# Performance work log

Hardware: AMD Instinct MI355X
Metric: run time of the kernel (lower is better)

The kernel has to match this reference:

```python
import jax, jax.numpy as jnp
import numpy as np

C1, C2, C3 = 64, 256, 256
HEADS, WS = 8, 7
HD = C3 // HEADS
PAD = WS // 2
SCALE = HD ** -0.5
EPS = 1e-5


def _layernorm(x, gamma, beta):
    mu = jnp.mean(x, axis=-1, keepdims=True)
    var = jnp.var(x, axis=-1, keepdims=True)
    return (x - mu) * jax.lax.rsqrt(var + EPS) * gamma + beta


def setup_inputs() -> dict:
    key = jax.random.key(0)
    ks = jax.random.split(key, 12)
    B, H, W = 2, 200, 200
    s = 0.02
    return {
        "F_lidar": jax.random.normal(ks[0], (B, C1, H, W), jnp.float32),
        "F_cam": jax.random.normal(ks[1], (B, C2, H, W), jnp.float32),
        "Wq": jax.random.normal(ks[2], (C3, C1), jnp.float32) * s,
        "Wk": jax.random.normal(ks[3], (C3, C2), jnp.float32) * s,
        "Wv": jax.random.normal(ks[4], (C3, C2), jnp.float32) * s,
        "Wo": jax.random.normal(ks[5], (C3, C3), jnp.float32) * s,
        "Wr": jax.random.normal(ks[6], (C3, C1), jnp.float32) * s,
        "g1": jnp.ones((C3,), jnp.float32),
        "b1": jnp.zeros((C3,), jnp.float32),
        "g2": jnp.ones((C3,), jnp.float32),
        "b2": jnp.zeros((C3,), jnp.float32),
        "W1": jax.random.normal(ks[7], (C3, 4 * C3), jnp.float32) * s,
        "bf1": jnp.zeros((4 * C3,), jnp.float32),
        "W2": jax.random.normal(ks[8], (4 * C3, C3), jnp.float32) * s,
        "bf2": jnp.zeros((C3,), jnp.float32),
    }


def reference(F_lidar, F_cam, Wq, Wk, Wv, Wo, Wr, g1, b1, g2, b2, W1, bf1, W2, bf2):
    B, _, H, W = F_lidar.shape
    # 1x1 conv projections (no bias)
    Q = jnp.einsum('oc,bchw->bohw', Wq, F_lidar)
    K = jnp.einsum('oc,bchw->bohw', Wk, F_cam)
    V = jnp.einsum('oc,bchw->bohw', Wv, F_cam)
    # replicate padding (torch 'replicate' == jnp 'edge')
    Kp = jnp.pad(K, ((0, 0), (0, 0), (PAD, PAD), (PAD, PAD)), mode='edge')
    Vp = jnp.pad(V, ((0, 0), (0, 0), (PAD, PAD), (PAD, PAD)), mode='edge')
    Qm = Q.reshape(B, HEADS, HD, H, W)
    # local-window attention logits without materializing the unfolded (C*49) tensor:
    # loop over the 49 fixed window offsets, accumulating per-offset dot products.
    logits = []
    for i in range(WS):
        for j in range(WS):
            Km = Kp[:, :, i:i + H, j:j + W].reshape(B, HEADS, HD, H, W)
            logits.append(jnp.einsum('bndhw,bndhw->bnhw', Qm, Km))
    logits = jnp.stack(logits, axis=-1) * SCALE          # (B, heads, H, W, 49)
    attn = jax.nn.softmax(logits, axis=-1)
    out = jnp.zeros_like(Qm)
    k = 0
    for i in range(WS):
        for j in range(WS):
            Vm = Vp[:, :, i:i + H, j:j + W].reshape(B, HEADS, HD, H, W)
            out = out + attn[..., k][:, :, None] * Vm
            k += 1
    out = out.reshape(B, C3, H, W)
    out = jnp.einsum('oc,bchw->bohw', Wo, out)
    residual = jnp.einsum('oc,bchw->bohw', Wr, F_lidar)
    x = (residual + out).transpose(0, 2, 3, 1)           # (B, H, W, C3)
    x = _layernorm(x, g1, b1)
    # FFN (dropout is identity in eval)
    y = jax.nn.relu(jnp.dot(x, W1) + bf1)
    y = jnp.dot(y, W2) + bf2
    x = _layernorm(x + y, g2, b2)
    return x.transpose(0, 3, 1, 2)
```

## Files before the change

### kernel.cpp

```cpp
#include <hip/hip_runtime.h>
#include <stdint.h>

#define HH 200
#define WW 200
#define HWSZ 40000
#define NPX 80000

typedef __attribute__((ext_vector_type(8))) short bf16x8;
typedef __attribute__((ext_vector_type(4))) float f32x4;

__device__ __forceinline__ float bf2f(unsigned short u) {
    union { uint32_t i; float f; } c; c.i = ((uint32_t)u) << 16; return c.f;
}
__device__ __forceinline__ unsigned short f2bf(float f) {
    union { float f; uint32_t i; } c; c.f = f;
    uint32_t r = c.i + 0x7FFF + ((c.i >> 16) & 1);
    return (unsigned short)(r >> 16);
}
__device__ __forceinline__ unsigned int cvtpk_bf16(float lo, float hi) {
    unsigned int r;
    asm("v_cvt_pk_bf16_f32 %0, %1, %2" : "=v"(r) : "v"(lo), "v"(hi));
    return r;
}

__global__ __launch_bounds__(256) void cvt_weights(
    const float* __restrict__ Wq, const float* __restrict__ Wk,
    const float* __restrict__ Wv, const float* __restrict__ Wo,
    const float* __restrict__ Wr, const float* __restrict__ W1,
    const float* __restrict__ W2,
    unsigned short* Wq_b, unsigned short* Wk_b, unsigned short* Wv_b,
    unsigned short* Wcat, unsigned short* W1t, unsigned short* W2t)
{
    const int seg = blockIdx.y;
    const int idx = blockIdx.x * 256 + threadIdx.x;
    if (seg == 0)      { if (idx < 16384) Wq_b[idx] = f2bf(Wq[idx]); }
    else if (seg == 1) { if (idx < 65536) Wk_b[idx] = f2bf(Wk[idx]); }
    else if (seg == 2) { if (idx < 65536) Wv_b[idx] = f2bf(Wv[idx]); }
    else if (seg == 3) {
        if (idx < 81920) {
            int r = idx / 320, k = idx - r * 320;
            Wcat[idx] = f2bf(k < 256 ? Wo[r * 256 + k] : Wr[r * 64 + (k - 256)]);
        }
    } else if (seg == 4) {
        if (idx < 262144) { int o = idx >> 8, i = idx & 255; W1t[idx] = f2bf(W1[i * 1024 + o]); }
    } else {
        if (idx < 262144) { int o = idx >> 10, i = idx & 1023; W2t[idx] = f2bf(W2[i * 256 + o]); }
    }
}

__global__ __launch_bounds__(256) void to_nhwc(
    const float* __restrict__ src, unsigned short* __restrict__ dst, int C)
{
    __shared__ unsigned short T[64][72];
    const int b = blockIdx.z, c0 = blockIdx.y * 64, px0 = blockIdx.x * 64;
    const int t = threadIdx.x;
    const int pxl = t & 63, cl0 = t >> 6;
    const float* sp = src + ((size_t)(b * C + c0 + cl0)) * HWSZ + px0 + pxl;
    #pragma unroll
    for (int i = 0; i < 16; ++i)
        T[pxl][cl0 + i * 4] = f2bf(sp[(size_t)i * 4 * HWSZ]);
    __syncthreads();
    #pragma unroll
    for (int r = 0; r < 2; ++r) {
        int idx = t + r * 256;
        int p = idx >> 3, cof = (idx & 7) * 8;
        uint4 v = *(const uint4*)&T[p][cof];
        *(uint4*)(dst + ((size_t)(b * HWSZ + px0 + p)) * C + c0 + cof) = v;
    }
}

__global__ __launch_bounds__(256) void gemm_bf16(
    const unsigned short* __restrict__ In, int inStride,
    const unsigned short* __restrict__ In2, int in2Stride, int K1,
    const unsigned short* __restrict__ Wb, int wStride, int Ktot,
    unsigned short* __restrict__ OutB, float* __restrict__ OutF,
    const float* __restrict__ bias, int flags, int outStride)
{
    __shared__ bf16x8 AB[1024];
    const int t = threadIdx.x;
    const int px0 = blockIdx.x * 128;
    const int n0 = blockIdx.y * 128;
    const int lane = t & 63, w = t >> 6;
    const int mh = w & 1, nh = w >> 1;

    f32x4 acc[4][4] = {};

    for (int k0 = 0; k0 < Ktot; k0 += 32) {
        #pragma unroll
        for (int r = 0; r < 2; ++r) {
            const int c = t + r * 256;
            const int l = c & 63;
            const int ko = k0 + ((l >> 4) << 3);
            {
                const int mt = c >> 6;
                const int px = px0 + mt * 16 + (l & 15);
                const unsigned short* sp = (ko < K1)
                    ? (In  + (size_t)px * inStride  + ko)
                    : (In2 + (size_t)px * in2Stride + (ko - K1));
                AB[c] = *(const bf16x8*)sp;
            }
            {
                const int nt = c >> 6;
                const int cc = n0 + nt * 16 + (l & 15);
                AB[512 + c] = *(const bf16x8*)(Wb + (size_t)cc * wStride + ko);
            }
        }
        __syncthreads();
        bf16x8 av[4], bv[4];
        #pragma unroll
        for (int i = 0; i < 4; ++i) av[i] = AB[(mh * 4 + i) * 64 + lane];
        #pragma unroll
        for (int j = 0; j < 4; ++j) bv[j] = AB[512 + (nh * 4 + j) * 64 + lane];
        #pragma unroll
        for (int i = 0; i < 4; ++i)
            #pragma unroll
            for (int j = 0; j < 4; ++j)
                acc[i][j] = __builtin_amdgcn_mfma_f32_16x16x32_bf16(
                    av[i], bv[j], acc[i][j], 0, 0, 0);
        __syncthreads();
    }

    const int q = lane >> 4, ln = lane & 15;
    const bool relu = (flags & 1) != 0, accum = (flags & 2) != 0;
    #pragma unroll
    for (int i = 0; i < 4; ++i) {
        #pragma unroll
        for (int j = 0; j < 4; ++j) {
            const int coutv = n0 + nh * 64 + j * 16 + ln;
            const float bval = bias ? bias[coutv] : 0.0f;
            #pragma unroll
            for (int r = 0; r < 4; ++r) {
                const int px = px0 + mh * 64 + i * 16 + q * 4 + r;
                float v = acc[i][j][r] + bval;
                if (relu) v = fmaxf(v, 0.0f);
                if (OutB) {
                    OutB[(size_t)px * outStride + coutv] = f2bf(v);
                } else {
                    float* op = OutF + (size_t)px * 256 + coutv;
                    if (accum) v += *op;
                    *op = v;
                }
            }
        }
    }
}

__global__ __launch_bounds__(512) void ffn2_ln2(
    const unsigned short* __restrict__ Y1,
    const unsigned short* __restrict__ XLb,
    const unsigned short* __restrict__ W2t,
    const float* __restrict__ bf2v,
    const float* __restrict__ g2, const float* __restrict__ b2,
    float* __restrict__ Out)
{
    __shared__ union {
        bf16x8 AB[1536];
        float  T[256 * 33];
    } sm;
    __shared__ float part_s[4][128], part_q[4][128];

    const int t = threadIdx.x;
    const int px0 = blockIdx.x * 128;
    const int lane = t & 63, w = t >> 6;
    const int mh = w & 1, nh = w >> 1;
    const int q = lane >> 4, ln = lane & 15;

    f32x4 acc[4][4] = {};

    for (int k0 = 0; k0 < 1024; k0 += 32) {
        #pragma unroll
        for (int r = 0; r < 3; ++r) {
            const int c = t + r * 512;
            const int l = c & 63;
            const int ko = k0 + ((l >> 4) << 3);
            if (c < 512) {
                const int mt = c >> 6;
                const int px = px0 + mt * 16 + (l & 15);
                sm.AB[c] = *(const bf16x8*)(Y1 + (size_t)px * 1024 + ko);
            } else {
                const int c2 = c - 512;
                const int nt = c2 >> 6;
                const int cc = nt * 16 + (l & 15);
                sm.AB[c] = *(const bf16x8*)(W2t + (size_t)cc * 1024 + ko);
            }
        }
        __syncthreads();
        bf16x8 av[4], bv[4];
        #pragma unroll
        for (int i = 0; i < 4; ++i) av[i] = sm.AB[(mh * 4 + i) * 64 + lane];
        #pragma unroll
        for (int j = 0; j < 4; ++j) bv[j] = sm.AB[512 + (nh * 4 + j) * 64 + lane];
        #pragma unroll
        for (int i = 0; i < 4; ++i)
            #pragma unroll
            for (int j = 0; j < 4; ++j)
                acc[i][j] = __builtin_amdgcn_mfma_f32_16x16x32_bf16(
                    av[i], bv[j], acc[i][j], 0, 0, 0);
        __syncthreads();
    }

    float biasv[4], gv[4], bvv[4];
    #pragma unroll
    for (int j = 0; j < 4; ++j) {
        const int col = nh * 64 + j * 16 + ln;
        biasv[j] = bf2v[col];
        gv[j] = g2[col];
        bvv[j] = b2[col];
    }

    #pragma unroll
    for (int i = 0; i < 4; ++i) {
        #pragma unroll
        for (int r = 0; r < 4; ++r) {
            const int pl = mh * 64 + i * 16 + q * 4 + r;
            const size_t px = (size_t)px0 + pl;
            float s = 0.0f, ssq = 0.0f;
            #pragma unroll
            for (int j = 0; j < 4; ++j) {
                const int col = nh * 64 + j * 16 + ln;
                float v = acc[i][j][r] + biasv[j] + bf2f(XLb[px * 256 + col]);
                acc[i][j][r] = v;
                s += v; ssq += v * v;
            }
            #pragma unroll
            for (int o = 1; o <= 8; o <<= 1) {
                s += __shfl_xor(s, o); ssq += __shfl_xor(ssq, o);
            }
            if (ln == 0) { part_s[nh][pl] = s; part_q[nh][pl] = ssq; }
        }
    }
    __syncthreads();

    float muv[4][4], rsv[4][4];
    #pragma unroll
    for (int i = 0; i < 4; ++i) {
        #pragma unroll
        for (int r = 0; r < 4; ++r) {
            const int pl = mh * 64 + i * 16 + q * 4 + r;
            const float s  = part_s[0][pl] + part_s[1][pl] + part_s[2][pl] + part_s[3][pl];
            const float sq = part_q[0][pl] + part_q[1][pl] + part_q[2][pl] + part_q[3][pl];
            const float mu = s * (1.0f / 256.0f);
            muv[i][r] = mu;
            rsv[i][r] = rsqrtf(sq * (1.0f / 256.0f) - mu * mu + 1e-5f);
        }
    }
    __syncthreads();

    #pragma unroll
    for (int ck = 0; ck < 4; ++ck) {
        if (mh == (ck >> 1)) {
            const int ib = (ck & 1) * 2;
            #pragma unroll
            for (int ii = 0; ii < 2; ++ii) {
                const int i = ib + ii;
                #pragma unroll
                for (int j = 0; j < 4; ++j) {
                    const int col = nh * 64 + j * 16 + ln;
                    #pragma unroll
                    for (int r = 0; r < 4; ++r) {
                        sm.T[col * 33 + ii * 16 + q * 4 + r] =
                            (acc[i][j][r] - muv[i][r]) * rsv[i][r] * gv[j] + bvv[j];
                    }
                }
            }
        }
        __syncthreads();
        const int pxc = px0 + ck * 32;
        const int bb = pxc / HWSZ;
        const int hw0 = pxc - bb * HWSZ;
        #pragma unroll
        for (int p = 0; p < 16; ++p) {
            const int idx = t + p * 512;
            const int c = idx >> 5, pxl = idx & 31;
            Out[((size_t)(bb * 256 + c)) * HWSZ + hw0 + pxl] = sm.T[c * 33 + pxl];
        }
        __syncthreads();
    }
}

__global__ __launch_bounds__(256) void attn_bf16(
    const unsigned short* Q, const unsigned short* __restrict__ K,
    const unsigned short* __restrict__ V, unsigned short* A)
{
    __shared__ __align__(16) unsigned short vt[32 * 536];
    const int b = blockIdx.z, head = blockIdx.y;
    const int tiy = blockIdx.x / 13, tix = blockIdx.x % 13;
    const int h0 = tiy * 16, w0 = tix * 16;
    const int t = threadIdx.x;
    const int lane = t & 63, wv = t >> 6;
    const int g = lane >> 4, n = lane & 15;
    const int co = head * 32;
    const size_t pxb = (size_t)b * HWSZ;

    for (int idx = t; idx < 832; idx += 256) {
        if (idx < 704) {
            int ch = idx / 22, r = idx - ch * 22;
            *(unsigned int*)&vt[ch * 536 + r * 24 + 22] = 0u;
        } else {
            int k2 = idx - 704;
            int ch = k2 >> 2, e = k2 & 3;
            *(unsigned int*)&vt[ch * 536 + 528 + e * 2] = 0u;
        }
    }
    for (int idx = t; idx < 484 * 4; idx += 256) {
        int pos = idx >> 2, chunk = idx & 3;
        int r = pos / 22, c = pos - r * 22;
        int gh = min(max(h0 + r - 3, 0), HH - 1);
        int gw = min(max(w0 + c - 3, 0), WW - 1);
        bf16x8 v8 = *(const bf16x8*)(V + (pxb + gh * WW + gw) * 256 + co + chunk * 8);
        unsigned short* dp = &vt[(chunk * 8) * 536 + r * 24 + c];
        #pragma unroll
        for (int e = 0; e < 8; ++e) dp[e * 536] = (unsigned short)v8[e];
    }
    __syncthreads();

    const f32x4 z4 = {0.f, 0.f, 0.f, 0.f};
    const int qw  = min(w0 + n, WW - 1);
    const int kc0 = min(max(w0 - 3 + n, 0), WW - 1);
    const int kc1 = min(w0 + 13 + n, WW - 1);
    const bool hi2 = (g >> 1) != 0;
    const int src0 = ((g & 1) * 2) * 16 + n;
    const int src1 = src0 + 16;

    for (int hh = 0; hh < 4; ++hh) {
        const int hl = wv * 4 + hh;
        const int h = h0 + hl;
        const int hc = min(h, HH - 1);

        const bf16x8 qf = *(const bf16x8*)(Q + (pxb + hc * WW + qw) * 256 + co + g * 8);

        f32x4 s0[7], s1[7];
        #pragma unroll
        for (int i = 0; i < 7; ++i) {
            const int gh = min(max(h - 3 + i, 0), HH - 1);
            const unsigned short* kr = K + (pxb + gh * WW) * 256 + co + g * 8;
            bf16x8 a0 = *(const bf16x8*)(kr + (size_t)kc0 * 256);
            bf16x8 a1 = *(const bf16x8*)(kr + (size_t)kc1 * 256);
            s0[i] = __builtin_amdgcn_mfma_f32_16x16x32_bf16(a0, qf, z4, 0, 0, 0);
            s1[i] = __builtin_amdgcn_mfma_f32_16x16x32_bf16(a1, qf, z4, 0, 0, 0);
        }

        float mx = -3.0e38f;
        #pragma unroll
        for (int r = 0; r < 4; ++r) {
            float m0 = s0[0][r], m1 = s1[0][r];
            #pragma unroll
            for (int i = 1; i < 7; ++i) {
                m0 = fmaxf(m0, s0[i][r]);
                m1 = fmaxf(m1, s1[i][r]);
            }
            const int k0 = 4 * g + r, k1 = k0 + 16;
            mx = fmaxf(mx, ((unsigned)(k0 - n) <= 6u) ? m0 : -3.0e38f);
            mx = fmaxf(mx, ((unsigned)(k1 - n) <= 6u) ? m1 : -3.0e38f);
        }
        mx = fmaxf(mx, __shfl_xor(mx, 16));
        mx = fmaxf(mx, __shfl_xor(mx, 32));

        float sum = 0.0f;
        #pragma unroll
        for (int r = 0; r < 4; ++r) {
            const int k0 = 4 * g + r, k1 = k0 + 16;
            const bool in0 = (unsigned)(k0 - n) <= 6u;
            const bool in1 = (unsigned)(k1 - n) <= 6u;
            #pragma unroll
            for (int i = 0; i < 7; ++i) {
                float e0 = in0 ? __expf((s0[i][r] - mx) * 0.17677669529663687f) : 0.0f;
                float e1 = in1 ? __expf((s1[i][r] - mx) * 0.17677669529663687f) : 0.0f;
                s0[i][r] = e0; s1[i][r] = e1;
                sum += e0 + e1;
            }
        }
        sum += __shfl_xor(sum, 16);
        sum += __shfl_xor(sum, 32);
        const float inv = __builtin_amdgcn_rcpf(sum);

        unsigned int pa[7], pb[7], pc[7], pd[7];
        #pragma unroll
        for (int i = 0; i < 7; ++i) {
            pa[i] = cvtpk_bf16(s0[i][0] * inv, s0[i][1] * inv);
            pb[i] = cvtpk_bf16(s0[i][2] * inv, s0[i][3] * inv);
            pc[i] = cvtpk_bf16(s1[i][0] * inv, s1[i][1] * inv);
            pd[i] = cvtpk_bf16(s1[i][2] * inv, s1[i][3] * inv);
        }

        f32x4 acc0 = z4, acc1 = z4;
        #pragma unroll
        for (int i = 0; i < 7; ++i) {
            const int a0s = __shfl((int)pa[i], src0);
            const int c0s = __shfl((int)pc[i], src0);
            const int b0s = __shfl((int)pb[i], src0);
            const int d0s = __shfl((int)pd[i], src0);
            const int a1s = __shfl((int)pa[i], src1);
            const int c1s = __shfl((int)pc[i], src1);
            const int b1s = __shfl((int)pb[i], src1);
            const int d1s = __shfl((int)pd[i], src1);
            union { unsigned int u[4]; bf16x8 v; } pu;
            pu.u[0] = (unsigned int)(hi2 ? c0s : a0s);
            pu.u[1] = (unsigned int)(hi2 ? d0s : b0s);
            pu.u[2] = (unsigned int)(hi2 ? c1s : a1s);
            pu.u[3] = (unsigned int)(hi2 ? d1s : b1s);
            const unsigned short* vr = &vt[(hl + i) * 24 + g * 8];
            bf16x8 vf0 = *(const bf16x8*)(vr + n * 536);
            bf16x8 vf1 = *(const bf16x8*)(vr + (n + 16) * 536);
            acc0 = __builtin_amdgcn_mfma_f32_16x16x32_bf16(pu.v, vf0, acc0, 0, 0, 0);
            acc1 = __builtin_amdgcn_mfma_f32_16x16x32_bf16(pu.v, vf1, acc1, 0, 0, 0);
        }

        if (h < HH) {
            unsigned short* ap = A + (pxb + h * WW) * 256 + co + n;
            const int wp = w0 + g * 4;
            #pragma unroll
            for (int r = 0; r < 4; ++r) {
                if (wp + r < WW) {
                    ap[(size_t)(wp + r) * 256]      = f2bf(acc0[r]);
                    ap[(size_t)(wp + r) * 256 + 16] = f2bf(acc1[r]);
                }
            }
        }
    }
}

__global__ __launch_bounds__(256) void ln1_k(
    const float* __restrict__ X, const float* __restrict__ g,
    const float* __restrict__ bt, unsigned short* __restrict__ XLb)
{
    const int wv = threadIdx.x >> 6, lane = threadIdx.x & 63;
    const size_t px = (size_t)blockIdx.x * 4 + wv;
    const float4 v = *(const float4*)(X + px * 256 + lane * 4);
    float s = v.x + v.y + v.z + v.w;
    float ss = v.x * v.x + v.y * v.y + v.z * v.z + v.w * v.w;
    #pragma unroll
    for (int o = 32; o; o >>= 1) { s += __shfl_xor(s, o); ss += __shfl_xor(ss, o); }
    const float mu = s * (1.0f / 256.0f);
    const float var = ss * (1.0f / 256.0f) - mu * mu;
    const float rs = rsqrtf(var + 1e-5f);
    const float4 gv = *(const float4*)(g + lane * 4);
    const float4 bv = *(const float4*)(bt + lane * 4);
    ushort4 o4;
    o4.x = f2bf((v.x - mu) * rs * gv.x + bv.x);
    o4.y = f2bf((v.y - mu) * rs * gv.y + bv.y);
    o4.z = f2bf((v.z - mu) * rs * gv.z + bv.z);
    o4.w = f2bf((v.w - mu) * rs * gv.w + bv.w);
    *(ushort4*)(XLb + px * 256 + lane * 4) = o4;
}

extern "C" void kernel_launch(void* const* d_in, const int* in_sizes, int n_in,
                              void* d_out, int out_size, void* d_ws, size_t ws_size,
                              hipStream_t stream)
{
    const float* F_lidar = (const float*)d_in[0];
    const float* F_cam   = (const float*)d_in[1];
    const float* Wq  = (const float*)d_in[2];
    const float* Wk  = (const float*)d_in[3];
    const float* Wv  = (const float*)d_in[4];
    const float* Wo  = (const float*)d_in[5];
    const float* Wr  = (const float*)d_in[6];
    const float* g1  = (const float*)d_in[7];
    const float* b1  = (const float*)d_in[8];
    const float* g2  = (const float*)d_in[9];
    const float* b2  = (const float*)d_in[10];
    const float* W1  = (const float*)d_in[11];
    const float* bf1 = (const float*)d_in[12];
    const float* W2  = (const float*)d_in[13];
    const float* bf2 = (const float*)d_in[14];

    char* wsb = (char*)d_ws;
    unsigned short* Fl  = (unsigned short*)(wsb);
    unsigned short* Fc  = (unsigned short*)(wsb + 10240000);
    unsigned short* Qb  = (unsigned short*)(wsb + 51200000);
    unsigned short* Kb  = (unsigned short*)(wsb + 92160000);
    unsigned short* Vb  = (unsigned short*)(wsb + 133120000);
    unsigned short* Y1b = Fc;
    unsigned short* XLb = (unsigned short*)(wsb + 174080000);
    unsigned short* Wq_b = (unsigned short*)(wsb + 215040000);
    unsigned short* Wk_b = Wq_b + 16384;
    unsigned short* Wv_b = Wk_b + 65536;
    unsigned short* Wcat = Wv_b + 65536;
    unsigned short* W1t  = Wcat + 81920;
    unsigned short* W2t  = W1t + 262144;
    float* XW  = (float*)d_out;
    float* out = (float*)d_out;

    const dim3 blk(256);

    cvt_weights<<<dim3(1024, 6), blk, 0, stream>>>(Wq, Wk, Wv, Wo, Wr, W1, W2,
        Wq_b, Wk_b, Wv_b, Wcat, W1t, W2t);
    to_nhwc<<<dim3(625, 1, 2), blk, 0, stream>>>(F_lidar, Fl, 64);
    to_nhwc<<<dim3(625, 4, 2), blk, 0, stream>>>(F_cam, Fc, 256);

    gemm_bf16<<<dim3(625, 2), blk, 0, stream>>>(Fl, 64, Fl, 64, 64,
        Wq_b, 64, 64, Qb, nullptr, nullptr, 0, 256);
    gemm_bf16<<<dim3(625, 2), blk, 0, stream>>>(Fc, 256, Fc, 256, 256,
        Wk_b, 256, 256, Kb, nullptr, nullptr, 0, 256);
    gemm_bf16<<<dim3(625, 2), blk, 0, stream>>>(Fc, 256, Fc, 256, 256,
        Wv_b, 256, 256, Vb, nullptr, nullptr, 0, 256);

    attn_bf16<<<dim3(169, 8, 2), blk, 0, stream>>>(Qb, Kb, Vb, Qb);

    gemm_bf16<<<dim3(625, 2), blk, 0, stream>>>(Qb, 256, Fl, 64, 256,
        Wcat, 320, 320, nullptr, XW, nullptr, 0, 256);

    ln1_k<<<dim3(20000), blk, 0, stream>>>(XW, g1, b1, XLb);

    gemm_bf16<<<dim3(625, 8), blk, 0, stream>>>(XLb, 256, XLb, 256, 256,
        W1t, 256, 256, Y1b, nullptr, bf1, 1, 1024);

    ffn2_ln2<<<dim3(625), dim3(512), 0, stream>>>(Y1b, XLb, W2t, bf2, g2, b2, out);
}
```

Baseline: 734.0 us.

## Use direct global-to-LDS loads and XCD-aware block remapping in GEMMs and attention

GEMM tile loads in gemm_bf16 and ffn2_ln2 now use global_load_lds, so data goes straight from global memory into LDS instead of passing through VGPRs. A new flag bit remaps block indices so that consecutive tiles land on the same XCD, which should improve L2 reuse of the shared input rows across the N tiles. The attention kernel applies a similar XCD-aware permutation that keeps the 16 head/batch blocks of one spatial tile together, so the overlapping K/V halos are shared in the same L2. The LDS layout assumption for direct loads (per-lane contiguous 16-byte placement) must match the existing layout or results break.

```diff
diff --git a/kernel.cpp b/kernel.cpp
--- a/kernel.cpp
+++ b/kernel.cpp
@@ -21,6 +21,11 @@
     unsigned int r;
     asm("v_cvt_pk_bf16_f32 %0, %1, %2" : "=v"(r) : "v"(lo), "v"(hi));
     return r;
+}
+__device__ __forceinline__ void gload16(const void* g, void* l) {
+    __builtin_amdgcn_global_load_lds(
+        (const __attribute__((address_space(1))) unsigned int*)g,
+        (__attribute__((address_space(3))) unsigned int*)l, 16, 0, 0);
 }
 
 __global__ __launch_bounds__(256) void cvt_weights(
@@ -78,8 +83,19 @@
 {
     __shared__ bf16x8 AB[1024];
     const int t = threadIdx.x;
-    const int px0 = blockIdx.x * 128;
-    const int n0 = blockIdx.y * 128;
+    int bx = blockIdx.x, by = blockIdx.y;
+    if (flags & 4) {
+        const int nxy = gridDim.x * gridDim.y;
+        const int flat = blockIdx.x + gridDim.x * blockIdx.y;
+        const int qq = nxy >> 3, rr = nxy & 7;
+        const int xcd = flat & 7, idx = flat >> 3;
+        const int w2 = (xcd < rr ? xcd * (qq + 1)
+                                 : rr * (qq + 1) + (xcd - rr) * qq) + idx;
+        by = w2 % gridDim.y;
+        bx = w2 / gridDim.y;
+    }
+    const int px0 = bx * 128;
+    const int n0 = by * 128;
     const int lane = t & 63, w = t >> 6;
     const int mh = w & 1, nh = w >> 1;
 
@@ -97,12 +113,12 @@
                 const unsigned short* sp = (ko < K1)
                     ? (In  + (size_t)px * inStride  + ko)
                     : (In2 + (size_t)px * in2Stride + (ko - K1));
-                AB[c] = *(const bf16x8*)sp;
+                gload16(sp, &AB[c]);
             }
             {
                 const int nt = c >> 6;
                 const int cc = n0 + nt * 16 + (l & 15);
-                AB[512 + c] = *(const bf16x8*)(Wb + (size_t)cc * wStride + ko);
+                gload16(Wb + (size_t)cc * wStride + ko, &AB[512 + c]);
             }
         }
         __syncthreads();
@@ -176,12 +192,12 @@
             if (c < 512) {
                 const int mt = c >> 6;
                 const int px = px0 + mt * 16 + (l & 15);
-                sm.AB[c] = *(const bf16x8*)(Y1 + (size_t)px * 1024 + ko);
+                gload16(Y1 + (size_t)px * 1024 + ko, &sm.AB[c]);
             } else {
                 const int c2 = c - 512;
                 const int nt = c2 >> 6;
                 const int cc = nt * 16 + (l & 15);
-                sm.AB[c] = *(const bf16x8*)(W2t + (size_t)cc * 1024 + ko);
+                gload16(W2t + (size_t)cc * 1024 + ko, &sm.AB[c]);
             }
         }
         __syncthreads();
@@ -283,8 +299,11 @@
     const unsigned short* __restrict__ V, unsigned short* A)
 {
     __shared__ __align__(16) unsigned short vt[32 * 536];
-    const int b = blockIdx.z, head = blockIdx.y;
-    const int tiy = blockIdx.x / 13, tix = blockIdx.x % 13;
+    const int flat = blockIdx.x + 169 * (blockIdx.y + 8 * blockIdx.z);
+    const int wsz = (flat & 7) * 338 + (flat >> 3);
+    const int tile = wsz >> 4, rem = wsz & 15;
+    const int head = rem >> 1, b = rem & 1;
+    const int tiy = tile / 13, tix = tile - tiy * 13;
     const int h0 = tiy * 16, w0 = tix * 16;
     const int t = threadIdx.x;
     const int lane = t & 63, wv = t >> 6;
@@ -489,21 +508,21 @@
     to_nhwc<<<dim3(625, 4, 2), blk, 0, stream>>>(F_cam, Fc, 256);
 
     gemm_bf16<<<dim3(625, 2), blk, 0, stream>>>(Fl, 64, Fl, 64, 64,
-        Wq_b, 64, 64, Qb, nullptr, nullptr, 0, 256);
+        Wq_b, 64, 64, Qb, nullptr, nullptr, 4, 256);
     gemm_bf16<<<dim3(625, 2), blk, 0, stream>>>(Fc, 256, Fc, 256, 256,
-        Wk_b, 256, 256, Kb, nullptr, nullptr, 0, 256);
+        Wk_b, 256, 256, Kb, nullptr, nullptr, 4, 256);
     gemm_bf16<<<dim3(625, 2), blk, 0, stream>>>(Fc, 256, Fc, 256, 256,
-        Wv_b, 256, 256, Vb, nullptr, nullptr, 0, 256);
+        Wv_b, 256, 256, Vb, nullptr, nullptr, 4, 256);
 
     attn_bf16<<<dim3(169, 8, 2), blk, 0, stream>>>(Qb, Kb, Vb, Qb);
 
     gemm_bf16<<<dim3(625, 2), blk, 0, stream>>>(Qb, 256, Fl, 64, 256,
-        Wcat, 320, 320, nullptr, XW, nullptr, 0, 256);
+        Wcat, 320, 320, nullptr, XW, nullptr, 4, 256);
 
     ln1_k<<<dim3(20000), blk, 0, stream>>>(XW, g1, b1, XLb);
 
     gemm_bf16<<<dim3(625, 8), blk, 0, stream>>>(XLb, 256, XLb, 256, 256,
-        W1t, 256, 256, Y1b, nullptr, bf1, 1, 1024);
+        W1t, 256, 256, Y1b, nullptr, bf1, 5, 1024);
 
     ffn2_ln2<<<dim3(625), dim3(512), 0, stream>>>(Y1b, XLb, W2t, bf2, g2, b2, out);
 }
```

After: 721.6 us. No clear change (-1.7%).
